# Optimization experiments

Measured on AMD Instinct MI355X. Metric: run time of the kernel, lower is better.

The kernel has to match this reference:

```python
import jax, jax.numpy as jnp
import numpy as np

S, B, C, H, W, N = 2, 16, 80, 128, 128, 128
HW = H * W
EPS = 1e-4
PULL_W = PUSH_W = OFF_W = 1.0


def _sig(x):
    return jnp.clip(jax.nn.sigmoid(x), EPS, 1.0 - EPS)


def _gather_feat(feat, ind):
    # feat [B,C,H,W], ind [B,N] flat HW indices -> [B,N,C]
    b, c = feat.shape[0], feat.shape[1]
    f = feat.transpose(0, 2, 3, 1).reshape(b, -1, c)
    idx = jnp.broadcast_to(ind[:, :, None], (b, ind.shape[1], c))
    return jnp.take_along_axis(f, idx, axis=1)


def _focal(pred, gt):
    pos = gt == 1.0
    neg = gt < 1.0
    negw = jnp.square(jnp.square(1.0 - gt))  # (1-gt)^4
    pos_loss = jnp.sum(jnp.where(pos, jnp.log(pred) * jnp.square(1.0 - pred), 0.0))
    neg_loss = jnp.sum(jnp.where(neg, jnp.log(1.0 - pred) * jnp.square(pred) * negw, 0.0))
    num_pos = jnp.sum(pos.astype(pred.dtype))
    return jnp.where(num_pos > 0, -(pos_loss + neg_loss) / num_pos, -neg_loss)


def _ae(tag0, tag1, mask):
    t0 = tag0[..., 0]  # [B,N]
    t1 = tag1[..., 0]
    m = mask.astype(t0.dtype)
    num = jnp.sum(m, axis=1, keepdims=True)  # [B,1]
    mean = (t0 + t1) * 0.5
    pull = jnp.sum(m * jnp.square(t0 - mean) / (num + EPS)) + \
           jnp.sum(m * jnp.square(t1 - mean) / (num + EPS))
    m2 = m[:, None, :] * m[:, :, None]  # [B,N,N] both-valid pairs
    numc = num[:, :, None]              # [B,1,1]
    num2 = (numc - 1.0) * numc
    dist = jax.nn.relu(1.0 - jnp.abs(mean[:, None, :] - mean[:, :, None]))
    dist = (dist - 1.0 / (numc + EPS)) / (num2 + EPS)
    push = jnp.sum(m2 * dist)
    return pull, push


def _off_loss(off, gt_off, mask):
    m = mask.astype(off.dtype)
    num = jnp.sum(m)
    d = jnp.abs(off - gt_off)
    sl1 = jnp.where(d < 1.0, 0.5 * d * d, d - 0.5)
    return jnp.sum(m[:, :, None] * sl1) / (num + EPS)


def setup_inputs() -> dict:
    key = jax.random.key(0)
    ks = jax.random.split(key, 20)

    def mk_gt(k):
        k1, k2 = jax.random.split(k)
        base = jax.random.uniform(k1, (B, C * H * W), jnp.float32) * 0.99
        idx = jax.random.randint(k2, (B, 64), 0, C * H * W)
        base = base.at[jnp.arange(B)[:, None], idx].set(1.0)
        return base.reshape(B, C, H, W)

    return {
        "tl_heats": jax.random.normal(ks[0], (S, B, C, H, W), jnp.float32),
        "br_heats": jax.random.normal(ks[1], (S, B, C, H, W), jnp.float32),
        "tl_tags": jax.random.normal(ks[2], (S, B, 1, H, W), jnp.float32),
        "br_tags": jax.random.normal(ks[3], (S, B, 1, H, W), jnp.float32),
        "tl_offs": jax.random.normal(ks[4], (S, B, 2, H, W), jnp.float32),
        "br_offs": jax.random.normal(ks[5], (S, B, 2, H, W), jnp.float32),
        "gt_tl_heat": mk_gt(ks[6]),
        "gt_br_heat": mk_gt(ks[7]),
        "gt_tag_mask": jax.random.bernoulli(ks[8], 0.5, (B, N)),
        "gt_off_tl_mask": jax.random.bernoulli(ks[9], 0.5, (B, N)),
        "gt_off_br_mask": jax.random.bernoulli(ks[10], 0.5, (B, N)),
        "gt_tl_off": jax.random.uniform(ks[11], (B, N, 2), jnp.float32),
        "gt_br_off": jax.random.uniform(ks[12], (B, N, 2), jnp.float32),
        "gt_tl_tag_ind": jax.random.randint(ks[13], (B, N), 0, HW),
        "gt_br_tag_ind": jax.random.randint(ks[14], (B, N), 0, HW),
        "gt_tl_off_ind": jax.random.randint(ks[15], (B, N), 0, HW),
        "gt_br_off_ind": jax.random.randint(ks[16], (B, N), 0, HW),
    }


def reference(tl_heats, br_heats, tl_tags, br_tags, tl_offs, br_offs,
              gt_tl_heat, gt_br_heat, gt_tag_mask, gt_off_tl_mask, gt_off_br_mask,
              gt_tl_off, gt_br_off, gt_tl_tag_ind, gt_br_tag_ind,
              gt_tl_off_ind, gt_br_off_ind):
    nstack = tl_heats.shape[0]
    focal = 0.0
    pull = 0.0
    push = 0.0
    off = 0.0
    for s in range(nstack):
        focal = focal + _focal(_sig(tl_heats[s]), gt_tl_heat)
        focal = focal + _focal(_sig(br_heats[s]), gt_br_heat)
        t0 = _gather_feat(tl_tags[s], gt_tl_tag_ind)
        t1 = _gather_feat(br_tags[s], gt_br_tag_ind)
        p, q = _ae(t0, t1, gt_tag_mask)
        pull = pull + p
        push = push + q
        o0 = _gather_feat(tl_offs[s], gt_tl_off_ind)
        o1 = _gather_feat(br_offs[s], gt_br_off_ind)
        off = off + _off_loss(o0, gt_tl_off, gt_off_tl_mask)
        off = off + _off_loss(o1, gt_br_off, gt_off_br_mask)
    loss = (focal + PULL_W * pull + PUSH_W * push + OFF_W * off) / max(nstack, 1)
    return loss[None]
```

## Files before the change

kernel.cpp:

```cpp
#include <hip/hip_runtime.h>
#include <math.h>

constexpr int S_ = 2, B_ = 16, C_ = 80, H_ = 128, W_ = 128, N_ = 128;
constexpr int HW_ = H_ * W_;
constexpr long long BCHW_ = (long long)B_ * C_ * HW_;
constexpr int NV4_ = (int)(BCHW_ / 4);
#define EPSF 1e-4f

constexpr int FOCAL_BPS = 1024;
constexpr int F4_PER_BLOCK = NV4_ / FOCAL_BPS;
constexpr int F4_PER_THREAD = F4_PER_BLOCK / 256;
constexpr int BATCH = 5;
constexpr int NBATCH = F4_PER_THREAD / BATCH;


__device__ inline float wave_reduce_sum(float v) {
#pragma unroll
  for (int off = 32; off > 0; off >>= 1) v += __shfl_down(v, off, 64);
  return v;
}

__device__ inline void focal_elem_bl(float x, bool pos, float negw,
                                     float& posacc, float& negacc) {
  float t = __expf(-x);
  float p = __builtin_amdgcn_rcpf(1.0f + t);
  p = fminf(fmaxf(p, 1e-4f), 1.0f - 1e-4f);
  float om = 1.0f - p;
  float lq = __logf(pos ? p : om);
  posacc += pos ? lq * (om * om) : 0.0f;
  negacc += pos ? 0.0f : lq * (p * p) * negw;
}

__device__ inline void focal4(const float4& g, const float4& a, const float4& b,
                              float& pacc, float& nacc, float& npos) {
  const float ge[4] = {g.x, g.y, g.z, g.w};
  const float ae[4] = {a.x, a.y, a.z, a.w};
  const float be[4] = {b.x, b.y, b.z, b.w};
#pragma unroll
  for (int k = 0; k < 4; ++k) {
    const float gv = ge[k];
    const bool pos = (gv == 1.0f);
    const float omg = 1.0f - gv;
    const float negw = (omg * omg) * (omg * omg);
    npos += pos ? 1.0f : 0.0f;
    focal_elem_bl(ae[k], pos, negw, pacc, nacc);
    focal_elem_bl(be[k], pos, negw, pacc, nacc);
  }
}

__global__ __launch_bounds__(256, 4) void focal_kernel(
    const float4* __restrict__ tl, const float4* __restrict__ br,
    const float4* __restrict__ gtl, const float4* __restrict__ gbr,
    float* __restrict__ ws) {
  const int slice = blockIdx.y;
  const float4* __restrict__ pred = (slice == 0) ? tl : br;
  const float4* __restrict__ gt = (slice == 0) ? gtl : gbr;

  float pacc = 0.0f, nacc = 0.0f, npos = 0.0f;

  int idx = blockIdx.x * F4_PER_BLOCK + threadIdx.x;

  for (int bt = 0; bt < NBATCH; ++bt) {
    float4 g[BATCH], a[BATCH], b[BATCH];
#pragma unroll
    for (int i = 0; i < BATCH; ++i) {
      const int j = idx + i * 256;
      g[i] = gt[j];
      a[i] = pred[j];
      b[i] = pred[NV4_ + j];
    }
#pragma unroll
    for (int i = 0; i < BATCH; ++i) {
      focal4(g[i], a[i], b[i], pacc, nacc, npos);
    }
    idx += BATCH * 256;
  }

  __shared__ float red[4][3];
  const int wave = threadIdx.x >> 6, lane = threadIdx.x & 63;
  float r0 = wave_reduce_sum(pacc);
  float r1 = wave_reduce_sum(nacc);
  float r2 = wave_reduce_sum(npos);
  if (lane == 0) { red[wave][0] = r0; red[wave][1] = r1; red[wave][2] = r2; }
  __syncthreads();
  if (threadIdx.x == 0) {
    float tp = red[0][0] + red[1][0] + red[2][0] + red[3][0];
    float tn = red[0][1] + red[1][1] + red[2][1] + red[3][1];
    float tc = red[0][2] + red[1][2] + red[2][2] + red[3][2];
    atomicAdd(&ws[0 + slice], tp);
    atomicAdd(&ws[2 + slice], tn);
    atomicAdd(&ws[4 + slice], tc);
  }
}

__device__ inline float sl1f(float d) {
  float a = fabsf(d);
  return (a < 1.0f) ? 0.5f * a * a : a - 0.5f;
}

__global__ __launch_bounds__(128) void ae_off_kernel(
    const float* __restrict__ tl_tags, const float* __restrict__ br_tags,
    const float* __restrict__ tl_offs, const float* __restrict__ br_offs,
    const int* __restrict__ tag_mask,
    const int* __restrict__ off_tl_mask, const int* __restrict__ off_br_mask,
    const float* __restrict__ gt_tl_off, const float* __restrict__ gt_br_off,
    const int* __restrict__ tl_tag_ind, const int* __restrict__ br_tag_ind,
    const int* __restrict__ tl_off_ind, const int* __restrict__ br_off_ind,
    float* __restrict__ ws) {
  const int s = blockIdx.x / B_;
  const int b = blockIdx.x % B_;
  const int n = threadIdx.x;

  __shared__ float sm_mean[N_];
  __shared__ float sm_m[N_];

  const float m = (tag_mask[b * N_ + n] != 0) ? 1.0f : 0.0f;
  const float t0 = tl_tags[(s * B_ + b) * HW_ + tl_tag_ind[b * N_ + n]];
  const float t1 = br_tags[(s * B_ + b) * HW_ + br_tag_ind[b * N_ + n]];
  const float mean = 0.5f * (t0 + t1);
  sm_mean[n] = mean;
  sm_m[n] = m;
  __syncthreads();

  float num = 0.0f;
  for (int j = 0; j < N_; ++j) num += sm_m[j];
  const float invn = 1.0f / (num + EPSF);
  const float d0 = t0 - mean, d1 = t1 - mean;
  const float pull_n = m * (d0 * d0 + d1 * d1) * invn;

  const float num2 = (num - 1.0f) * num;
  const float inv2 = 1.0f / (num2 + EPSF);
  float pacc = 0.0f;
  for (int j = 0; j < N_; ++j) {
    float dd = 1.0f - fabsf(mean - sm_mean[j]);
    dd = fmaxf(dd, 0.0f);
    pacc += sm_m[j] * (dd - invn);
  }
  const float push_n = m * pacc * inv2;

  const float mo_tl = (off_tl_mask[b * N_ + n] != 0) ? 1.0f : 0.0f;
  const float mo_br = (off_br_mask[b * N_ + n] != 0) ? 1.0f : 0.0f;
  const int io0 = tl_off_ind[b * N_ + n];
  const int io1 = br_off_ind[b * N_ + n];
  const float o00 = tl_offs[((s * B_ + b) * 2 + 0) * HW_ + io0];
  const float o01 = tl_offs[((s * B_ + b) * 2 + 1) * HW_ + io0];
  const float o10 = br_offs[((s * B_ + b) * 2 + 0) * HW_ + io1];
  const float o11 = br_offs[((s * B_ + b) * 2 + 1) * HW_ + io1];
  const float g00 = gt_tl_off[(b * N_ + n) * 2 + 0];
  const float g01 = gt_tl_off[(b * N_ + n) * 2 + 1];
  const float g10 = gt_br_off[(b * N_ + n) * 2 + 0];
  const float g11 = gt_br_off[(b * N_ + n) * 2 + 1];
  const float sl_tl = mo_tl * (sl1f(o00 - g00) + sl1f(o01 - g01));
  const float sl_br = mo_br * (sl1f(o10 - g10) + sl1f(o11 - g11));

  float vals[6] = {pull_n, push_n, sl_tl, sl_br,
                   (s == 0) ? mo_tl : 0.0f, (s == 0) ? mo_br : 0.0f};
  __shared__ float red[2][6];
  const int wave = n >> 6, lane = n & 63;
#pragma unroll
  for (int k = 0; k < 6; ++k) {
    float r = wave_reduce_sum(vals[k]);
    if (lane == 0) red[wave][k] = r;
  }
  __syncthreads();
  if (n == 0) {
    atomicAdd(&ws[10 + s], red[0][0] + red[1][0]);
    atomicAdd(&ws[12 + s], red[0][1] + red[1][1]);
    atomicAdd(&ws[14 + s], red[0][2] + red[1][2]);
    atomicAdd(&ws[16 + s], red[0][3] + red[1][3]);
    atomicAdd(&ws[18], red[0][4] + red[1][4]);
    atomicAdd(&ws[19], red[0][5] + red[1][5]);
  }
}

__global__ void finalize_kernel(const float* __restrict__ ws,
                                float* __restrict__ out) {
  if (threadIdx.x == 0 && blockIdx.x == 0) {
    const float npos_tl = ws[4], npos_br = ws[5];
    float focal = 0.0f;
    focal += (npos_tl > 0.0f) ? -(ws[0] + ws[2]) / npos_tl : -ws[2];
    focal += (npos_br > 0.0f) ? -(ws[1] + ws[3]) / npos_br : -ws[3];
    const float pull = ws[10] + ws[11];
    const float push = ws[12] + ws[13];
    const float off = (ws[14] + ws[15]) / (ws[18] + EPSF) +
                      (ws[16] + ws[17]) / (ws[19] + EPSF);
    out[0] = (focal + pull + push + off) * 0.5f;
  }
}

extern "C" void kernel_launch(void* const* d_in, const int* in_sizes, int n_in,
                              void* d_out, int out_size, void* d_ws, size_t ws_size,
                              hipStream_t stream) {
  const float* tl_heats   = (const float*)d_in[0];
  const float* br_heats   = (const float*)d_in[1];
  const float* tl_tags    = (const float*)d_in[2];
  const float* br_tags    = (const float*)d_in[3];
  const float* tl_offs    = (const float*)d_in[4];
  const float* br_offs    = (const float*)d_in[5];
  const float* gt_tl_heat = (const float*)d_in[6];
  const float* gt_br_heat = (const float*)d_in[7];
  const int* gt_tag_mask    = (const int*)d_in[8];
  const int* gt_off_tl_mask = (const int*)d_in[9];
  const int* gt_off_br_mask = (const int*)d_in[10];
  const float* gt_tl_off  = (const float*)d_in[11];
  const float* gt_br_off  = (const float*)d_in[12];
  const int* gt_tl_tag_ind = (const int*)d_in[13];
  const int* gt_br_tag_ind = (const int*)d_in[14];
  const int* gt_tl_off_ind = (const int*)d_in[15];
  const int* gt_br_off_ind = (const int*)d_in[16];

  float* ws = (float*)d_ws;
  float* out = (float*)d_out;

  hipMemsetAsync(ws, 0, 32 * sizeof(float), stream);

  dim3 fgrid(FOCAL_BPS, 2, 1);
  focal_kernel<<<fgrid, 256, 0, stream>>>(
      (const float4*)tl_heats, (const float4*)br_heats,
      (const float4*)gt_tl_heat, (const float4*)gt_br_heat, ws);

  ae_off_kernel<<<S_ * B_, N_, 0, stream>>>(
      tl_tags, br_tags, tl_offs, br_offs,
      gt_tag_mask, gt_off_tl_mask, gt_off_br_mask,
      gt_tl_off, gt_br_off,
      gt_tl_tag_ind, gt_br_tag_ind, gt_tl_off_ind, gt_br_off_ind, ws);

  finalize_kernel<<<1, 64, 0, stream>>>(ws, out);
}
```

Before: 487.9 us.

## Double-buffer focal loads, rewrite sigmoid-log math, fuse finalize into AE kernel

The focal kernel now prefetches the next batch of gt and prediction loads into a second register buffer while the current batch is computed, with a scheduling barrier between the two, and launch bounds are relaxed to allow more registers. Per-element math is restructured to compute a single exp and log via log(1+e^-x), replacing the branchy select-based accumulation with predicated multiply-adds. The finalize kernel is removed; the last AE block, detected through an atomic counter, computes the final loss. The gains sought are hiding memory latency and saving one launch. The costs are higher register pressure and lower occupancy, and the clamp-based log identity only approximates the original probability clipping.

```diff
diff --git a/kernel.cpp b/kernel.cpp
--- a/kernel.cpp
+++ b/kernel.cpp
@@ -10,8 +10,10 @@
 constexpr int FOCAL_BPS = 1024;
 constexpr int F4_PER_BLOCK = NV4_ / FOCAL_BPS;
 constexpr int F4_PER_THREAD = F4_PER_BLOCK / 256;
-constexpr int BATCH = 5;
+constexpr int BATCH = 4;
 constexpr int NBATCH = F4_PER_THREAD / BATCH;
+
+#define CLAMP_C 9.2102404f
 
 
 __device__ inline float wave_reduce_sum(float v) {
@@ -20,15 +22,18 @@
   return v;
 }
 
-__device__ inline void focal_elem_bl(float x, bool pos, float negw,
-                                     float& posacc, float& negacc) {
-  float t = __expf(-x);
-  float p = __builtin_amdgcn_rcpf(1.0f + t);
-  p = fminf(fmaxf(p, 1e-4f), 1.0f - 1e-4f);
-  float om = 1.0f - p;
-  float lq = __logf(pos ? p : om);
-  posacc += pos ? lq * (om * om) : 0.0f;
-  negacc += pos ? 0.0f : lq * (p * p) * negw;
+__device__ inline void focal_elem2(float x, float wpos, float wneg, float negw,
+                                   float& pacc, float& nacc) {
+  float xc = fminf(fmaxf(-x, -CLAMP_C), CLAMP_C);
+  float t = __expf(xc);
+  float u = 1.0f + t;
+  float p = __builtin_amdgcn_rcpf(u);
+  float l1 = __logf(u);
+  float om = t * p;
+  float posv = l1 * om * om;
+  float negv = (l1 - xc) * p * p * negw;
+  pacc = fmaf(wpos, posv, pacc);
+  nacc = fmaf(wneg, negv, nacc);
 }
 
 __device__ inline void focal4(const float4& g, const float4& a, const float4& b,
@@ -39,16 +44,17 @@
 #pragma unroll
   for (int k = 0; k < 4; ++k) {
     const float gv = ge[k];
-    const bool pos = (gv == 1.0f);
+    const float wpos = (gv == 1.0f) ? 1.0f : 0.0f;
+    const float wneg = 1.0f - wpos;
     const float omg = 1.0f - gv;
     const float negw = (omg * omg) * (omg * omg);
-    npos += pos ? 1.0f : 0.0f;
-    focal_elem_bl(ae[k], pos, negw, pacc, nacc);
-    focal_elem_bl(be[k], pos, negw, pacc, nacc);
-  }
-}
-
-__global__ __launch_bounds__(256, 4) void focal_kernel(
+    npos += wpos;
+    focal_elem2(ae[k], wpos, wneg, negw, pacc, nacc);
+    focal_elem2(be[k], wpos, wneg, negw, pacc, nacc);
+  }
+}
+
+__global__ __launch_bounds__(256, 2) void focal_kernel(
     const float4* __restrict__ tl, const float4* __restrict__ br,
     const float4* __restrict__ gtl, const float4* __restrict__ gbr,
     float* __restrict__ ws) {
@@ -58,22 +64,36 @@
 
   float pacc = 0.0f, nacc = 0.0f, npos = 0.0f;
 
-  int idx = blockIdx.x * F4_PER_BLOCK + threadIdx.x;
-
+  const int idx = blockIdx.x * F4_PER_BLOCK + threadIdx.x;
+
+  float4 bg[2][BATCH], ba[2][BATCH], bb[2][BATCH];
+
+#pragma unroll
+  for (int i = 0; i < BATCH; ++i) {
+    const int j = idx + i * 256;
+    bg[0][i] = gt[j];
+    ba[0][i] = pred[j];
+    bb[0][i] = pred[NV4_ + j];
+  }
+
+#pragma unroll
   for (int bt = 0; bt < NBATCH; ++bt) {
-    float4 g[BATCH], a[BATCH], b[BATCH];
+    const int cur = bt & 1, nxt = cur ^ 1;
+    if (bt + 1 < NBATCH) {
+      const int base = idx + (bt + 1) * (BATCH * 256);
+#pragma unroll
+      for (int i = 0; i < BATCH; ++i) {
+        const int j = base + i * 256;
+        bg[nxt][i] = gt[j];
+        ba[nxt][i] = pred[j];
+        bb[nxt][i] = pred[NV4_ + j];
+      }
+    }
+    __builtin_amdgcn_sched_barrier(0);
 #pragma unroll
     for (int i = 0; i < BATCH; ++i) {
-      const int j = idx + i * 256;
-      g[i] = gt[j];
-      a[i] = pred[j];
-      b[i] = pred[NV4_ + j];
+      focal4(bg[cur][i], ba[cur][i], bb[cur][i], pacc, nacc, npos);
     }
-#pragma unroll
-    for (int i = 0; i < BATCH; ++i) {
-      focal4(g[i], a[i], b[i], pacc, nacc, npos);
-    }
-    idx += BATCH * 256;
   }
 
   __shared__ float red[4][3];
@@ -106,7 +126,7 @@
     const float* __restrict__ gt_tl_off, const float* __restrict__ gt_br_off,
     const int* __restrict__ tl_tag_ind, const int* __restrict__ br_tag_ind,
     const int* __restrict__ tl_off_ind, const int* __restrict__ br_off_ind,
-    float* __restrict__ ws) {
+    float* __restrict__ ws, float* __restrict__ out) {
   const int s = blockIdx.x / B_;
   const int b = blockIdx.x % B_;
   const int n = threadIdx.x;
@@ -170,21 +190,24 @@
     atomicAdd(&ws[16 + s], red[0][3] + red[1][3]);
     atomicAdd(&ws[18], red[0][4] + red[1][4]);
     atomicAdd(&ws[19], red[0][5] + red[1][5]);
-  }
-}
-
-__global__ void finalize_kernel(const float* __restrict__ ws,
-                                float* __restrict__ out) {
-  if (threadIdx.x == 0 && blockIdx.x == 0) {
-    const float npos_tl = ws[4], npos_br = ws[5];
-    float focal = 0.0f;
-    focal += (npos_tl > 0.0f) ? -(ws[0] + ws[2]) / npos_tl : -ws[2];
-    focal += (npos_br > 0.0f) ? -(ws[1] + ws[3]) / npos_br : -ws[3];
-    const float pull = ws[10] + ws[11];
-    const float push = ws[12] + ws[13];
-    const float off = (ws[14] + ws[15]) / (ws[18] + EPSF) +
-                      (ws[16] + ws[17]) / (ws[19] + EPSF);
-    out[0] = (focal + pull + push + off) * 0.5f;
+
+    __threadfence();
+    unsigned int prev =
+        atomicAdd(reinterpret_cast<unsigned int*>(ws + 31), 1u);
+    if (prev == (unsigned int)(S_ * B_ - 1)) {
+      auto rd = [&](int i) { return atomicAdd(&ws[i], 0.0f); };
+      const float npos_tl = rd(4), npos_br = rd(5);
+      float focal = 0.0f;
+      const float p_tl = rd(0), n_tl = rd(2);
+      const float p_br = rd(1), n_br = rd(3);
+      focal += (npos_tl > 0.0f) ? (p_tl + n_tl) / npos_tl : n_tl;
+      focal += (npos_br > 0.0f) ? (p_br + n_br) / npos_br : n_br;
+      const float pull = rd(10) + rd(11);
+      const float push = rd(12) + rd(13);
+      const float off = (rd(14) + rd(15)) / (rd(18) + EPSF) +
+                        (rd(16) + rd(17)) / (rd(19) + EPSF);
+      out[0] = (focal + pull + push + off) * 0.5f;
+    }
   }
 }
 
@@ -223,7 +246,5 @@
       tl_tags, br_tags, tl_offs, br_offs,
       gt_tag_mask, gt_off_tl_mask, gt_off_br_mask,
       gt_tl_off, gt_br_off,
-      gt_tl_tag_ind, gt_br_tag_ind, gt_tl_off_ind, gt_br_off_ind, ws);
-
-  finalize_kernel<<<1, 64, 0, stream>>>(ws, out);
-}
+      gt_tl_tag_ind, gt_br_tag_ind, gt_tl_off_ind, gt_br_off_ind, ws, out);
+}
```

Result: no change. 492.8 us (+1.0%).
